# Kernel tuning notes

Measured on AMD Instinct MI355X. Metric: run time of the kernel, lower is better.

Reference implementation:

```python
import jax, jax.numpy as jnp
import numpy as np
import math

V, D, H, NL, ML = 30000, 1024, 16, 6, 1024
B, L = 2, 1024
DH = D // H
HID = D // 2  # BoundaryLayer hidden_dim = d_model // 2


def _ln(x, g, b):
    # torch LayerNorm: biased variance, eps=1e-5
    m = x.mean(-1, keepdims=True)
    v = jnp.var(x, axis=-1, keepdims=True)
    return (x - m) * jax.lax.rsqrt(v + 1e-5) * g + b


def setup_inputs() -> dict:
    key = jax.random.key(0)
    ks = iter(jax.random.split(key, 64))
    nrm = lambda shape, std=0.02: jax.random.normal(next(ks), shape, jnp.float32) * std

    def xav(shape):
        # xavier_uniform over last two dims (fan_in, fan_out) per layer
        fan_in, fan_out = shape[-2], shape[-1]
        bound = math.sqrt(6.0 / (fan_in + fan_out))
        return jax.random.uniform(next(ks), shape, jnp.float32, -bound, bound)

    inp = {
        "ids": jax.random.randint(next(ks), (B, L), 0, V),
        "embed": nrm((V, D)),              # tied with head
        "pos_enc": nrm((1, ML, D)),
        # per-layer stacked params
        "rg_w": nrm((NL, D, 4)),
        "rg_b": jnp.zeros((NL, 4)),
        "qkv_w": xav((NL, D, 3 * D)),
        "qkv_b": jnp.zeros((NL, 3 * D)),
        "out_w": xav((NL, D, D)),
        "out_b": jnp.zeros((NL, D)),
        "ph_w": xav((NL, D, H)),
        "ph_b": jnp.zeros((NL, H)),
        "res_scale": jnp.full((NL,), 0.1, jnp.float32),
        "ph_scale": jnp.ones((NL,), jnp.float32),
        "ff1_w": xav((NL, D, 4 * D)),
        "ff1_b": jnp.zeros((NL, 4 * D)),
        "ff2_w": xav((NL, 4 * D, D)),
        "ff2_b": jnp.zeros((NL, D)),
        "n1_g": jnp.ones((NL, D)),
        "n1_b": jnp.zeros((NL, D)),
        "n2_g": jnp.ones((NL, D)),
        "n2_b": jnp.zeros((NL, D)),
        # shared boundary MLP
        "bnd_w1": xav((D, HID)),
        "bnd_b1": jnp.zeros((HID,)),
        "bnd_w2": xav((HID, 1)),
        "bnd_b2": jnp.zeros((1,)),
        "fn_g": jnp.ones((D,)),
        "fn_b": jnp.zeros((D,)),
    }
    return inp


def reference(ids, embed, pos_enc, rg_w, rg_b, qkv_w, qkv_b, out_w, out_b,
              ph_w, ph_b, res_scale, ph_scale, ff1_w, ff1_b, ff2_w, ff2_b,
              n1_g, n1_b, n2_g, n2_b, bnd_w1, bnd_b1, bnd_w2, bnd_b2, fn_g, fn_b):
    b, l = ids.shape
    d = embed.shape[1]
    nl = rg_w.shape[0]
    h = ph_w.shape[-1]
    dh = d // h

    x = embed[ids] * math.sqrt(d) + pos_enc[:, :l, :]
    grammar, shocks = [], []
    for i in range(nl):
        # R-Grammar modulation
        rg = jax.nn.sigmoid(x @ rg_w[i] + rg_b[i])                  # [B,L,4]
        grammar.append(rg)
        xm = x * (1.0 + 0.1 * rg.mean(-1, keepdims=True))
        # resonance attention (pre-norm)
        a_in = _ln(xm, n1_g[i], n1_b[i])
        qkv = (a_in @ qkv_w[i] + qkv_b[i]).reshape(b, l, 3, h, dh)
        qkv = jnp.transpose(qkv, (2, 0, 3, 1, 4))                   # [3,B,H,L,dh]
        q, k, v = qkv[0], qkv[1], qkv[2]
        scores = jnp.einsum('bhld,bhmd->bhlm', q, k) / math.sqrt(dh)
        pv = jnp.tanh(ph_scale[i] * (a_in @ ph_w[i] + ph_b[i]))     # [B,L,H]
        pv = jnp.transpose(pv, (0, 2, 1))                           # [B,H,L]
        phase_diff = (pv[..., :, None] - pv[..., None, :]) ** 2     # [B,H,L,L]
        scores = scores - res_scale[i] * phase_diff
        aw = jax.nn.softmax(scores, axis=-1)
        o = jnp.einsum('bhlm,bhmd->bhld', aw, v)
        o = jnp.transpose(o, (0, 2, 1, 3)).reshape(b, l, d)
        x = xm + (o @ out_w[i] + out_b[i])
        # feed-forward (exact GELU, matching torch default)
        f_in = _ln(x, n2_g[i], n2_b[i])
        ff = jax.nn.gelu(f_in @ ff1_w[i] + ff1_b[i], approximate=False) @ ff2_w[i] + ff2_b[i]
        x = x + ff
        # boundary shock score (shared MLP)
        shock = jax.nn.sigmoid(jnp.tanh(x @ bnd_w1 + bnd_b1) @ bnd_w2 + bnd_b2)  # [B,L,1]
        shocks.append(shock)
    x = _ln(x, fn_g, fn_b)
    logits = x @ embed.T                                            # tied head
    gs = jnp.stack(grammar, 0)   # [NL,B,L,4]
    ss = jnp.stack(shocks, 0)    # [NL,B,L,1]
    return (logits, x, gs.mean(0), ss.mean(0), gs, ss)
```

## Files before the change

kernel.cpp:

```cpp
#include <hip/hip_runtime.h>
#include <math.h>

constexpr int NLAYER = 6;
constexpr int B_ = 2;
constexpr int L_ = 1024;
constexpr int D_ = 1024;
constexpr int H_ = 16;
constexpr int DH_ = 64;
constexpr int V_ = 30000;
constexpr int HID_ = 512;
constexpr int BL_ = B_ * L_;

typedef __bf16 bf16_t;
typedef bf16_t bf16x8 __attribute__((ext_vector_type(8)));
typedef bf16_t bf16x4 __attribute__((ext_vector_type(4)));
typedef float  f32x4  __attribute__((ext_vector_type(4)));

#define GLOAD_LDS16(gp, lp)                                                    \
    __builtin_amdgcn_global_load_lds(                                          \
        (const __attribute__((address_space(1))) void*)(gp),                   \
        (__attribute__((address_space(3))) void*)(lp), 16, 0, 0)

__device__ __forceinline__ float sigmoidf_(float z) { return 1.0f / (1.0f + expf(-z)); }
__device__ __forceinline__ float gelu_exact_(float z) {
    return 0.5f * z * (1.0f + erff(z * 0.70710678118654752440f));
}

__device__ __forceinline__ bf16x8 pack8_(const float* __restrict__ src) {
    float4 f0 = *(const float4*)(src);
    float4 f1 = *(const float4*)(src + 4);
    bf16x8 v;
    v[0] = (bf16_t)f0.x; v[1] = (bf16_t)f0.y; v[2] = (bf16_t)f0.z; v[3] = (bf16_t)f0.w;
    v[4] = (bf16_t)f1.x; v[5] = (bf16_t)f1.y; v[6] = (bf16_t)f1.z; v[7] = (bf16_t)f1.w;
    return v;
}

__device__ __forceinline__ float block_sum_(float v, float* red) {
    int tid = threadIdx.x;
    red[tid] = v; __syncthreads();
    #pragma unroll
    for (int s = 128; s > 0; s >>= 1) {
        if (tid < s) red[tid] += red[tid + s];
        __syncthreads();
    }
    float r = red[0];
    __syncthreads();
    return r;
}

__global__ __launch_bounds__(256) void embed_k(
    const int* __restrict__ ids, const float* __restrict__ emb,
    const float* __restrict__ pos, float* __restrict__ x)
{
    int t = blockIdx.x, tid = threadIdx.x;
    int id = ids[t];
    int l = t % L_;
    #pragma unroll
    for (int it = 0; it < 4; ++it) {
        int d = it * 256 + tid;
        x[(size_t)t * D_ + d] = emb[(size_t)id * D_ + d] * 32.0f + pos[(size_t)l * D_ + d];
    }
}

__global__ __launch_bounds__(256) void tcw_k(
    const float* s0, bf16_t* d0, int K0, int N0, int c0,
    const float* s1, bf16_t* d1, int K1, int N1, int c1,
    const float* s2, bf16_t* d2, int K2, int N2, int c2,
    const float* s3, bf16_t* d3, int K3, int N3, int c3)
{
    __shared__ float t32[32][33];
    int bid = blockIdx.x;
    const float* s; bf16_t* d; int K, N, base;
    if (bid < c0)      { s = s0; d = d0; K = K0; N = N0; base = 0; }
    else if (bid < c1) { s = s1; d = d1; K = K1; N = N1; base = c0; }
    else if (bid < c2) { s = s2; d = d2; K = K2; N = N2; base = c1; }
    else               { s = s3; d = d3; K = K3; N = N3; base = c2; }
    int tt = bid - base;
    int KT = K >> 5;
    int kt = tt % KT, nt = tt / KT;
    int tid = threadIdx.x, cx = tid & 31, ry = tid >> 5;
    #pragma unroll
    for (int j = 0; j < 4; ++j)
        t32[ry + 8 * j][cx] = s[(size_t)(kt * 32 + ry + 8 * j) * N + nt * 32 + cx];
    __syncthreads();
    #pragma unroll
    for (int j = 0; j < 4; ++j)
        d[(size_t)(nt * 32 + ry + 8 * j) * K + kt * 32 + cx] =
            (bf16_t)t32[cx][ry + 8 * j];
}

__global__ __launch_bounds__(256) void cvtb_k(
    const float* __restrict__ s, bf16_t* __restrict__ d, int n8)
{
    for (int i = blockIdx.x * 256 + threadIdx.x; i < n8; i += gridDim.x * 256)
        *(bf16x8*)(d + (size_t)i * 8) = pack8_(s + (size_t)i * 8);
}

__global__ __launch_bounds__(256) void rg_xm_ln_k(
    const float* __restrict__ x, const float* __restrict__ rgw,
    const float* __restrict__ rgb, const float* __restrict__ g,
    const float* __restrict__ b, const float* __restrict__ phw,
    const float* __restrict__ phb, const float* __restrict__ ps_p,
    float* __restrict__ xm, bf16_t* __restrict__ ainb,
    float* __restrict__ pvb, float* __restrict__ gs_out)
{
    int t = blockIdx.x, tid = threadIdx.x;
    __shared__ float xr[D_];
    __shared__ float red[256];
    __shared__ float rgsh[4];

    #pragma unroll
    for (int it = 0; it < 4; ++it) {
        int d = it * 256 + tid;
        xr[d] = x[(size_t)t * D_ + d];
    }
    __syncthreads();

    float a0 = 0.f, a1 = 0.f, a2 = 0.f, a3 = 0.f;
    #pragma unroll
    for (int it = 0; it < 4; ++it) {
        int d = it * 256 + tid;
        float xv = xr[d];
        float4 w = *(const float4*)(rgw + (size_t)d * 4);
        a0 += xv * w.x; a1 += xv * w.y; a2 += xv * w.z; a3 += xv * w.w;
    }
    float s0 = block_sum_(a0, red);
    float s1 = block_sum_(a1, red);
    float s2 = block_sum_(a2, red);
    float s3 = block_sum_(a3, red);
    if (tid == 0) {
        float r0 = sigmoidf_(s0 + rgb[0]);
        float r1 = sigmoidf_(s1 + rgb[1]);
        float r2 = sigmoidf_(s2 + rgb[2]);
        float r3 = sigmoidf_(s3 + rgb[3]);
        rgsh[0] = r0; rgsh[1] = r1; rgsh[2] = r2; rgsh[3] = r3;
        gs_out[(size_t)t * 4 + 0] = r0;
        gs_out[(size_t)t * 4 + 1] = r1;
        gs_out[(size_t)t * 4 + 2] = r2;
        gs_out[(size_t)t * 4 + 3] = r3;
    }
    __syncthreads();
    float factor = 1.0f + 0.025f * (rgsh[0] + rgsh[1] + rgsh[2] + rgsh[3]);

    float sm = 0.f, sq = 0.f;
    float vals[4];
    #pragma unroll
    for (int it = 0; it < 4; ++it) {
        int d = it * 256 + tid;
        float v = xr[d] * factor;
        vals[it] = v;
        xm[(size_t)t * D_ + d] = v;
        sm += v; sq += v * v;
    }
    float mean = block_sum_(sm, red) * (1.0f / D_);
    float msq  = block_sum_(sq, red) * (1.0f / D_);
    float rstd = rsqrtf(msq - mean * mean + 1e-5f);
    #pragma unroll
    for (int it = 0; it < 4; ++it) {
        int d = it * 256 + tid;
        float a = (vals[it] - mean) * rstd * g[d] + b[d];
        ainb[(size_t)t * D_ + d] = (bf16_t)a;
        xr[d] = a;
    }
    __syncthreads();

    {
        int c = tid & 15, grp = tid >> 4;
        float acc = 0.f;
        int k0 = grp * 64;
        #pragma unroll
        for (int kk = 0; kk < 64; ++kk)
            acc += xr[k0 + kk] * phw[(size_t)(k0 + kk) * H_ + c];
        red[tid] = acc;
        __syncthreads();
        if (tid < 16) {
            float s = 0.f;
            #pragma unroll
            for (int gg = 0; gg < 16; ++gg) s += red[gg * 16 + tid];
            pvb[(size_t)t * H_ + tid] = tanhf(ps_p[0] * (s + phb[tid]));
        }
    }
}

__global__ __launch_bounds__(256) void ln_k(
    const float* __restrict__ in, const float* __restrict__ g,
    const float* __restrict__ b, float* __restrict__ outp,
    bf16_t* __restrict__ outb)
{
    int t = blockIdx.x, tid = threadIdx.x;
    __shared__ float red[256];
    float s1 = 0.f, s2 = 0.f;
    float vals[4];
    #pragma unroll
    for (int it = 0; it < 4; ++it) {
        int d = it * 256 + tid;
        float v = in[(size_t)t * D_ + d];
        vals[it] = v; s1 += v; s2 += v * v;
    }
    float mean = block_sum_(s1, red) * (1.0f / D_);
    float msq  = block_sum_(s2, red) * (1.0f / D_);
    float rstd = rsqrtf(msq - mean * mean + 1e-5f);
    #pragma unroll
    for (int it = 0; it < 4; ++it) {
        int d = it * 256 + tid;
        float v = (vals[it] - mean) * rstd * g[d] + b[d];
        if (outp) outp[(size_t)t * D_ + d] = v;
        if (outb) outb[(size_t)t * D_ + d] = (bf16_t)v;
    }
}

template<int BN>
__global__ __launch_bounds__(256) void gemm_bf_k(
    const bf16_t* __restrict__ A, const bf16_t* __restrict__ Bm,
    const float* __restrict__ bias, const float* __restrict__ resid,
    float* __restrict__ C, bf16_t* __restrict__ Cb,
    int M, int N, int K, int MT, int GW,
    int act, const float* __restrict__ scale_ptr)
{
    constexpr int BM = 128;
    constexpr int BK = 64;
    constexpr int WN = BN / 32;

    __shared__ alignas(16) bf16_t As[BM][BK];
    __shared__ alignas(16) bf16_t Bs[BN][BK];

    const int tid  = threadIdx.x;
    const int lane = tid & 63;
    const int w    = tid >> 6;

    int per = MT * GW;
    int grp = blockIdx.x / per;
    int r   = blockIdx.x % per;
    int mi  = r % MT;
    int ni  = grp * GW + r / MT;
    const int bm = mi * BM;
    const int bn = ni * BN;

    const int wr = (w & 1) * 64;
    const int wc = (w >> 1) * (BN / 2);
    const int rlo = lane & 15, lhi = lane >> 4;
    const int srow = lane >> 3;
    const int scol = (lane & 7) * 8;

    f32x4 acc[4][WN];
    #pragma unroll
    for (int m = 0; m < 4; ++m)
        #pragma unroll
        for (int n = 0; n < WN; ++n) {
            f32x4 z = {0.f, 0.f, 0.f, 0.f};
            acc[m][n] = z;
        }

    for (int kt = 0; kt < K; kt += BK) {
        __syncthreads();
        #pragma unroll
        for (int i = 0; i < 4; ++i) {
            int is = w * 4 + i;
            const bf16_t* gp = A + (size_t)(bm + is * 8 + srow) * K + kt + scol;
            GLOAD_LDS16(gp, &As[is * 8][0]);
        }
        #pragma unroll
        for (int i = 0; i < BN / 32; ++i) {
            int is = w * (BN / 32) + i;
            int row = bn + is * 8 + srow;
            if (row > N - 1) row = N - 1;
            const bf16_t* gp = Bm + (size_t)row * K + kt + scol;
            GLOAD_LDS16(gp, &Bs[is * 8][0]);
        }
        __syncthreads();

        #pragma unroll
        for (int h2 = 0; h2 < 2; ++h2) {
            int ko = h2 * 32 + lhi * 8;
            bf16x8 af[4], bfr[WN];
            #pragma unroll
            for (int m = 0; m < 4; ++m)
                af[m] = *(const bf16x8*)(&As[wr + m * 16 + rlo][ko]);
            #pragma unroll
            for (int n = 0; n < WN; ++n)
                bfr[n] = *(const bf16x8*)(&Bs[wc + n * 16 + rlo][ko]);
            #pragma unroll
            for (int m = 0; m < 4; ++m)
                #pragma unroll
                for (int n = 0; n < WN; ++n)
                    acc[m][n] = __builtin_amdgcn_mfma_f32_16x16x32_bf16(
                        af[m], bfr[n], acc[m][n], 0, 0, 0);
        }
    }

    float scale = scale_ptr ? scale_ptr[0] : 1.0f;
    #pragma unroll
    for (int m = 0; m < 4; ++m) {
        #pragma unroll
        for (int n = 0; n < WN; ++n) {
            int col = bn + wc + n * 16 + rlo;
            if (col >= N) continue;
            #pragma unroll
            for (int i = 0; i < 4; ++i) {
                int row = bm + wr + m * 16 + lhi * 4 + i;
                float v = acc[m][n][i];
                if (bias) v += bias[col];
                if (act == 1)      v = gelu_exact_(v);
                else if (act == 2) v = tanhf(scale * v);
                if (resid) v += resid[(size_t)row * N + col];
                if (C)  C[(size_t)row * N + col] = v;
                if (Cb) Cb[(size_t)row * N + col] = (bf16_t)v;
            }
        }
    }
}

__global__ __launch_bounds__(256) void attn_mfma_k(
    const bf16_t* __restrict__ qkv, const float* __restrict__ pv,
    const float* __restrict__ res_scale_p, bf16_t* __restrict__ o)
{
    constexpr int QB = 64;
    constexpr int NB = 64;

    __shared__ alignas(16) bf16_t Ks[NB][DH_];
    __shared__ alignas(16) bf16_t Vt[DH_][NB];
    __shared__ alignas(16) bf16_t Pl[4][16][NB];
    __shared__ float pvq_s[QB];
    __shared__ float pvk_s[NB];

    const int qt = blockIdx.x, h = blockIdx.y, b = blockIdx.z;
    const int tid = threadIdx.x;
    const int lane = tid & 63, w = tid >> 6;
    const int rlo = lane & 15, lhi = lane >> 4, l7 = lane & 7;
    const float rs = res_scale_p[0];

    const size_t rowbase = (size_t)(b * L_ + qt * QB);

    bf16x8 qf[2];
    {
        const bf16_t* qrow = qkv + (rowbase + w * 16 + rlo) * 3072 + h * DH_;
        #pragma unroll
        for (int kk = 0; kk < 2; ++kk)
            qf[kk] = *(const bf16x8*)(qrow + kk * 32 + lhi * 8);
    }
    if (tid < QB) pvq_s[tid] = pv[(rowbase + tid) * H_ + h];

    float m_r[4], l_r[4];
    f32x4 acc_o[4];
    #pragma unroll
    for (int r = 0; r < 4; ++r) { m_r[r] = -1e30f; l_r[r] = 0.f; }
    #pragma unroll
    for (int n = 0; n < 4; ++n) {
        f32x4 z = {0.f, 0.f, 0.f, 0.f};
        acc_o[n] = z;
    }

    bf16_t* pw = &Pl[w][0][0];

    for (int k0 = 0; k0 < L_; k0 += NB) {
        __syncthreads();
        #pragma unroll
        for (int i = 0; i < 2; ++i) {
            int sid = i * 256 + tid;
            int row = sid >> 3, s = sid & 7;
            bf16x8 v = *(const bf16x8*)(qkv + (size_t)(b * L_ + k0 + row) * 3072
                                        + 1024 + h * DH_ + s * 8);
            *(bf16x8*)(&Ks[row][(s ^ (row & 7)) * 8]) = v;
        }
        {
            int col4 = (tid & 15) * 4;
            int kb   = tid >> 4;
            bf16x4 rv[4];
            #pragma unroll
            for (int j = 0; j < 4; ++j)
                rv[j] = *(const bf16x4*)(qkv + (size_t)(b * L_ + k0 + kb * 4 + j) * 3072
                                         + 2048 + h * DH_ + col4);
            #pragma unroll
            for (int jj = 0; jj < 4; ++jj) {
                int col = col4 + jj;
                bf16x4 v;
                #pragma unroll
                for (int j = 0; j < 4; ++j)
                    v[j] = rv[j][jj];
                *(bf16x4*)(&Vt[col][((kb >> 1) ^ (col & 7)) * 8 + (kb & 1) * 4]) = v;
            }
        }
        if (tid < NB) pvk_s[tid] = pv[(size_t)(b * L_ + k0 + tid) * H_ + h];
        __syncthreads();

        f32x4 sacc[4];
        #pragma unroll
        for (int n = 0; n < 4; ++n) {
            f32x4 z = {0.f, 0.f, 0.f, 0.f};
            sacc[n] = z;
        }
        #pragma unroll
        for (int kk = 0; kk < 2; ++kk) {
            int soff = ((kk * 4 + lhi) ^ l7) * 8;
            bf16x8 kf[4];
            #pragma unroll
            for (int n = 0; n < 4; ++n)
                kf[n] = *(const bf16x8*)(&Ks[n * 16 + rlo][soff]);
            #pragma unroll
            for (int n = 0; n < 4; ++n)
                sacc[n] = __builtin_amdgcn_mfma_f32_16x16x32_bf16(
                    qf[kk], kf[n], sacc[n], 0, 0, 0);
        }

        float sv[4][4];
        float tmax[4] = {-1e30f, -1e30f, -1e30f, -1e30f};
        #pragma unroll
        for (int n = 0; n < 4; ++n) {
            float pvk = pvk_s[n * 16 + rlo];
            #pragma unroll
            for (int r = 0; r < 4; ++r) {
                float dd = pvq_s[w * 16 + lhi * 4 + r] - pvk;
                float s = sacc[n][r] * 0.125f - rs * dd * dd;
                sv[n][r] = s;
                tmax[r] = fmaxf(tmax[r], s);
            }
        }
        #pragma unroll
        for (int st = 1; st < 16; st <<= 1)
            #pragma unroll
            for (int r = 0; r < 4; ++r)
                tmax[r] = fmaxf(tmax[r], __shfl_xor(tmax[r], st));

        float tsum[4] = {0.f, 0.f, 0.f, 0.f};
        #pragma unroll
        for (int r = 0; r < 4; ++r) {
            float mn = fmaxf(m_r[r], tmax[r]);
            float sc = expf(m_r[r] - mn);
            m_r[r] = mn;
            l_r[r] *= sc;
            #pragma unroll
            for (int n = 0; n < 4; ++n) acc_o[n][r] *= sc;
        }
        #pragma unroll
        for (int n = 0; n < 4; ++n) {
            int key = n * 16 + rlo;
            #pragma unroll
            for (int r = 0; r < 4; ++r) {
                float p = expf(sv[n][r] - m_r[r]);
                tsum[r] += p;
                int q = lhi * 4 + r;
                pw[q * NB + (((key >> 3) ^ (q & 7)) * 8 + (key & 7))] = (bf16_t)p;
            }
        }
        #pragma unroll
        for (int st = 1; st < 16; st <<= 1)
            #pragma unroll
            for (int r = 0; r < 4; ++r)
                tsum[r] += __shfl_xor(tsum[r], st);
        #pragma unroll
        for (int r = 0; r < 4; ++r) l_r[r] += tsum[r];

        #pragma unroll
        for (int kk = 0; kk < 2; ++kk) {
            int soff = ((kk * 4 + lhi) ^ l7) * 8;
            bf16x8 pa = *(const bf16x8*)(pw + rlo * NB + (((kk * 4 + lhi) ^ (rlo & 7)) * 8));
            bf16x8 vf[4];
            #pragma unroll
            for (int n = 0; n < 4; ++n)
                vf[n] = *(const bf16x8*)(&Vt[n * 16 + rlo][soff]);
            #pragma unroll
            for (int n = 0; n < 4; ++n)
                acc_o[n] = __builtin_amdgcn_mfma_f32_16x16x32_bf16(
                    pa, vf[n], acc_o[n], 0, 0, 0);
        }
    }

    float inv[4];
    #pragma unroll
    for (int r = 0; r < 4; ++r) inv[r] = 1.0f / l_r[r];
    #pragma unroll
    for (int n = 0; n < 4; ++n)
        #pragma unroll
        for (int r = 0; r < 4; ++r)
            o[(rowbase + w * 16 + lhi * 4 + r) * D_ + h * DH_ + n * 16 + rlo] =
                (bf16_t)(acc_o[n][r] * inv[r]);
}

__global__ __launch_bounds__(256) void bnd2_k(
    const float* __restrict__ hbuf, const float* __restrict__ w2,
    const float* __restrict__ b2, float* __restrict__ ss_out)
{
    int t = blockIdx.x, tid = threadIdx.x;
    __shared__ float red[256];
    float acc = 0.f;
    #pragma unroll
    for (int it = 0; it < 2; ++it) {
        int d = it * 256 + tid;
        acc += hbuf[(size_t)t * HID_ + d] * w2[d];
    }
    float s = block_sum_(acc, red);
    if (tid == 0) ss_out[t] = sigmoidf_(s + b2[0]);
}

__global__ __launch_bounds__(256) void means_k(
    const float* __restrict__ gs, const float* __restrict__ ss,
    float* __restrict__ gsm, float* __restrict__ ssm)
{
    int i = blockIdx.x * 256 + threadIdx.x;
    if (i < BL_ * 4) {
        float s = 0.f;
        #pragma unroll
        for (int l = 0; l < NLAYER; ++l) s += gs[(size_t)l * BL_ * 4 + i];
        gsm[i] = s * (1.0f / NLAYER);
    }
    if (i < BL_) {
        float s = 0.f;
        #pragma unroll
        for (int l = 0; l < NLAYER; ++l) s += ss[(size_t)l * BL_ + i];
        ssm[i] = s * (1.0f / NLAYER);
    }
}

extern "C" void kernel_launch(void* const* d_in, const int* in_sizes, int n_in,
                              void* d_out, int out_size, void* d_ws, size_t ws_size,
                              hipStream_t stream) {
    const int*   ids       = (const int*)  d_in[0];
    const float* embed     = (const float*)d_in[1];
    const float* pos_enc   = (const float*)d_in[2];
    const float* rg_w      = (const float*)d_in[3];
    const float* rg_b      = (const float*)d_in[4];
    const float* qkv_w     = (const float*)d_in[5];
    const float* qkv_b     = (const float*)d_in[6];
    const float* out_w     = (const float*)d_in[7];
    const float* out_b     = (const float*)d_in[8];
    const float* ph_w      = (const float*)d_in[9];
    const float* ph_b      = (const float*)d_in[10];
    const float* res_scale = (const float*)d_in[11];
    const float* ph_scale  = (const float*)d_in[12];
    const float* ff1_w     = (const float*)d_in[13];
    const float* ff1_b     = (const float*)d_in[14];
    const float* ff2_w     = (const float*)d_in[15];
    const float* ff2_b     = (const float*)d_in[16];
    const float* n1_g      = (const float*)d_in[17];
    const float* n1_b      = (const float*)d_in[18];
    const float* n2_g      = (const float*)d_in[19];
    const float* n2_b      = (const float*)d_in[20];
    const float* bnd_w1    = (const float*)d_in[21];
    const float* bnd_b1    = (const float*)d_in[22];
    const float* bnd_w2    = (const float*)d_in[23];
    const float* bnd_b2    = (const float*)d_in[24];
    const float* fn_g      = (const float*)d_in[25];
    const float* fn_b      = (const float*)d_in[26];

    float* out = (float*)d_out;
    float* ws  = (float*)d_ws;

    const size_t M1 = 1024 * 1024;
    float*  x    = ws;
    float*  xm   = ws + 2 * M1;
    float*  bndh = ws + 4 * M1;
    float*  pvb  = ws + 5 * M1;
    bf16_t* ainb = (bf16_t*)(ws + 5 * M1 + M1 / 4);
    bf16_t* aob  = (bf16_t*)(ws + 6 * M1 + M1 / 4);
    bf16_t* xb   = (bf16_t*)(ws + 7 * M1 + M1 / 4);
    bf16_t* qkvb = (bf16_t*)(ws + 8 * M1 + M1 / 4);
    bf16_t* ffhb = (bf16_t*)(ws + 11 * M1 + M1 / 4);
    float*  wT   = ws + 15 * M1 + M1 / 4;
    bf16_t* qkvT = (bf16_t*)(wT);
    bf16_t* outT = (bf16_t*)(wT + 1572864);
    bf16_t* ff1T = (bf16_t*)(wT + 2097152);
    bf16_t* ff2T = (bf16_t*)(wT + 4194304);
    bf16_t* bndT = (bf16_t*)(wT + 6291456);
    bf16_t* embB = qkvb;

    const size_t o_logits = 0;
    const size_t o_x      = (size_t)BL_ * V_;
    const size_t o_gsm    = o_x + (size_t)BL_ * D_;
    const size_t o_ssm    = o_gsm + (size_t)BL_ * 4;
    const size_t o_gs     = o_ssm + (size_t)BL_;
    const size_t o_ss     = o_gs + (size_t)NLAYER * BL_ * 4;

    embed_k<<<BL_, 256, 0, stream>>>(ids, embed, pos_enc, x);

    tcw_k<<<512, 256, 0, stream>>>(
        bnd_w1, bndT, D_, HID_, 512,
        bnd_w1, bndT, D_, HID_, 512,
        bnd_w1, bndT, D_, HID_, 512,
        bnd_w1, bndT, D_, HID_, 512);

    const int MT = BL_ / 128;

    for (int i = 0; i < NLAYER; ++i) {
        tcw_k<<<12288, 256, 0, stream>>>(
            qkv_w + (size_t)i * D_ * 3 * D_,    qkvT, D_,     3 * D_, 3072,
            out_w + (size_t)i * D_ * D_,        outT, D_,     D_,     4096,
            ff1_w + (size_t)i * D_ * 4 * D_,    ff1T, D_,     4 * D_, 8192,
            ff2_w + (size_t)i * 4 * D_ * D_,    ff2T, 4 * D_, D_,     12288);

        rg_xm_ln_k<<<BL_, 256, 0, stream>>>(
            x, rg_w + (size_t)i * D_ * 4, rg_b + (size_t)i * 4,
            n1_g + (size_t)i * D_, n1_b + (size_t)i * D_,
            ph_w + (size_t)i * D_ * H_, ph_b + (size_t)i * H_, ph_scale + i,
            xm, ainb, pvb, out + o_gs + (size_t)i * BL_ * 4);

        gemm_bf_k<128><<<MT * 24, 256, 0, stream>>>(
            ainb, qkvT, qkv_b + (size_t)i * 3 * D_, nullptr,
            nullptr, qkvb, BL_, 3 * D_, D_, MT, 4, 0, nullptr);

        dim3 ga(L_ / 64, H_, B_);
        attn_mfma_k<<<ga, 256, 0, stream>>>(qkvb, pvb, res_scale + i, aob);

        gemm_bf_k<64><<<MT * 16, 256, 0, stream>>>(
            aob, outT, out_b + (size_t)i * D_, xm,
            x, nullptr, BL_, D_, D_, MT, 4, 0, nullptr);

        ln_k<<<BL_, 256, 0, stream>>>(x, n2_g + (size_t)i * D_, n2_b + (size_t)i * D_,
                                      nullptr, ainb);

        gemm_bf_k<128><<<MT * 32, 256, 0, stream>>>(
            ainb, ff1T, ff1_b + (size_t)i * 4 * D_, nullptr,
            nullptr, ffhb, BL_, 4 * D_, D_, MT, 4, 1, nullptr);

        gemm_bf_k<64><<<MT * 16, 256, 0, stream>>>(
            ffhb, ff2T, ff2_b + (size_t)i * D_, x,
            x, xb, BL_, D_, 4 * D_, MT, 4, 0, nullptr);

        gemm_bf_k<64><<<MT * 8, 256, 0, stream>>>(
            xb, bndT, bnd_b1, nullptr,
            bndh, nullptr, BL_, HID_, D_, MT, 4, 2, nullptr);

        bnd2_k<<<BL_, 256, 0, stream>>>(bndh, bnd_w2, bnd_b2, out + o_ss + (size_t)i * BL_);
    }

    ln_k<<<BL_, 256, 0, stream>>>(x, fn_g, fn_b, out + o_x, xb);

    cvtb_k<<<4096, 256, 0, stream>>>(embed, embB, V_ * D_ / 8);

    gemm_bf_k<128><<<MT * 235, 256, 0, stream>>>(
        xb, embB, nullptr, nullptr,
        out + o_logits, nullptr, BL_, V_, D_, MT, 5, 0, nullptr);

    means_k<<<(BL_ * 4 + 255) / 256, 256, 0, stream>>>(
        out + o_gs, out + o_ss, out + o_gsm, out + o_ssm);
}
```

Measured before the change: 2.659 ms.

## Use fast exp/tanh intrinsics, hoist pvq to registers, vectorize transpose stores, add setprio

Replaces expf with __expf in attention softmax and sigmoid, and swaps tanhf for a custom exp-based tanh in the phase projection and GEMM epilogue. Loads the per-query phase values into registers once instead of rereading shared memory each tile. Writes the weight transpose as 4-wide bf16 vectors instead of scalar stores, and raises wave priority around the MFMA sections in attention. These trim transcendental and memory-instruction cost, at some loss of accuracy from the fast exp paths.

```diff
diff --git a/kernel.cpp b/kernel.cpp
--- a/kernel.cpp
+++ b/kernel.cpp
@@ -21,7 +21,13 @@
         (const __attribute__((address_space(1))) void*)(gp),                   \
         (__attribute__((address_space(3))) void*)(lp), 16, 0, 0)
 
-__device__ __forceinline__ float sigmoidf_(float z) { return 1.0f / (1.0f + expf(-z)); }
+__device__ __forceinline__ float sigmoidf_(float z) { return 1.0f / (1.0f + __expf(-z)); }
+__device__ __forceinline__ float tanhf_(float z) {
+    float a = fabsf(z);
+    float e = __expf(-2.0f * a);
+    float r = (1.0f - e) / (1.0f + e);
+    return copysignf(r, z);
+}
 __device__ __forceinline__ float gelu_exact_(float z) {
     return 0.5f * z * (1.0f + erff(z * 0.70710678118654752440f));
 }
@@ -83,10 +89,11 @@
     for (int j = 0; j < 4; ++j)
         t32[ry + 8 * j][cx] = s[(size_t)(kt * 32 + ry + 8 * j) * N + nt * 32 + cx];
     __syncthreads();
-    #pragma unroll
-    for (int j = 0; j < 4; ++j)
-        d[(size_t)(nt * 32 + ry + 8 * j) * K + kt * 32 + cx] =
-            (bf16_t)t32[cx][ry + 8 * j];
+    int r = tid >> 3, c4 = (tid & 7) * 4;
+    bf16x4 v;
+    #pragma unroll
+    for (int j = 0; j < 4; ++j) v[j] = (bf16_t)t32[c4 + j][r];
+    *(bf16x4*)(d + (size_t)(nt * 32 + r) * K + kt * 32 + c4) = v;
 }
 
 __global__ __launch_bounds__(256) void cvtb_k(
@@ -177,7 +184,7 @@
             float s = 0.f;
             #pragma unroll
             for (int gg = 0; gg < 16; ++gg) s += red[gg * 16 + tid];
-            pvb[(size_t)t * H_ + tid] = tanhf(ps_p[0] * (s + phb[tid]));
+            pvb[(size_t)t * H_ + tid] = tanhf_(ps_p[0] * (s + phb[tid]));
         }
     }
 }
@@ -301,7 +308,7 @@
                 float v = acc[m][n][i];
                 if (bias) v += bias[col];
                 if (act == 1)      v = gelu_exact_(v);
-                else if (act == 2) v = tanhf(scale * v);
+                else if (act == 2) v = tanhf_(scale * v);
                 if (resid) v += resid[(size_t)row * N + col];
                 if (C)  C[(size_t)row * N + col] = v;
                 if (Cb) Cb[(size_t)row * N + col] = (bf16_t)v;
@@ -339,6 +346,10 @@
             qf[kk] = *(const bf16x8*)(qrow + kk * 32 + lhi * 8);
     }
     if (tid < QB) pvq_s[tid] = pv[(rowbase + tid) * H_ + h];
+    __syncthreads();
+    float pvq_r[4];
+    #pragma unroll
+    for (int r = 0; r < 4; ++r) pvq_r[r] = pvq_s[w * 16 + lhi * 4 + r];
 
     float m_r[4], l_r[4];
     f32x4 acc_o[4];
@@ -389,6 +400,7 @@
             f32x4 z = {0.f, 0.f, 0.f, 0.f};
             sacc[n] = z;
         }
+        __builtin_amdgcn_s_setprio(1);
         #pragma unroll
         for (int kk = 0; kk < 2; ++kk) {
             int soff = ((kk * 4 + lhi) ^ l7) * 8;
@@ -401,6 +413,7 @@
                 sacc[n] = __builtin_amdgcn_mfma_f32_16x16x32_bf16(
                     qf[kk], kf[n], sacc[n], 0, 0, 0);
         }
+        __builtin_amdgcn_s_setprio(0);
 
         float sv[4][4];
         float tmax[4] = {-1e30f, -1e30f, -1e30f, -1e30f};
@@ -409,7 +422,7 @@
             float pvk = pvk_s[n * 16 + rlo];
             #pragma unroll
             for (int r = 0; r < 4; ++r) {
-                float dd = pvq_s[w * 16 + lhi * 4 + r] - pvk;
+                float dd = pvq_r[r] - pvk;
                 float s = sacc[n][r] * 0.125f - rs * dd * dd;
                 sv[n][r] = s;
                 tmax[r] = fmaxf(tmax[r], s);
@@ -425,7 +438,7 @@
         #pragma unroll
         for (int r = 0; r < 4; ++r) {
             float mn = fmaxf(m_r[r], tmax[r]);
-            float sc = expf(m_r[r] - mn);
+            float sc = __expf(m_r[r] - mn);
             m_r[r] = mn;
             l_r[r] *= sc;
             #pragma unroll
@@ -436,7 +449,7 @@
             int key = n * 16 + rlo;
             #pragma unroll
             for (int r = 0; r < 4; ++r) {
-                float p = expf(sv[n][r] - m_r[r]);
+                float p = __expf(sv[n][r] - m_r[r]);
                 tsum[r] += p;
                 int q = lhi * 4 + r;
                 pw[q * NB + (((key >> 3) ^ (q & 7)) * 8 + (key & 7))] = (bf16_t)p;
@@ -450,6 +463,7 @@
         #pragma unroll
         for (int r = 0; r < 4; ++r) l_r[r] += tsum[r];
 
+        __builtin_amdgcn_s_setprio(1);
         #pragma unroll
         for (int kk = 0; kk < 2; ++kk) {
             int soff = ((kk * 4 + lhi) ^ l7) * 8;
@@ -463,6 +477,7 @@
                 acc_o[n] = __builtin_amdgcn_mfma_f32_16x16x32_bf16(
                     pa, vf[n], acc_o[n], 0, 0, 0);
         }
+        __builtin_amdgcn_s_setprio(0);
     }
 
     float inv[4];
```

Result: faster. 2.587 ms (-2.7%).
